# Optimization experiments

Hardware: AMD Instinct MI355X
Metric: run time of the kernel (lower is better)

Reference implementation:

```python
import jax, jax.numpy as jnp
import numpy as np

N_NODES = 50000
N_EDGES = 800000
IN_CH, HID_CH, OUT_CH = 128, 128, 64


def gcn_conv(x, edge_index, edge_weight, W, b, n_nodes):
    """PyG GCNConv: h = D^-1/2 (A + I) D^-1/2 (x @ W) + b, with weighted edges."""
    src, dst = edge_index[0], edge_index[1]
    loop = jnp.arange(n_nodes)
    src_l = jnp.concatenate([src, loop])               # [E+N]
    dst_l = jnp.concatenate([dst, loop])               # [E+N]
    w_l = jnp.concatenate([edge_weight, jnp.ones((n_nodes,), x.dtype)])
    deg = jax.ops.segment_sum(w_l, dst_l, num_segments=n_nodes)  # weighted in-degree incl. self-loop
    dinv = jnp.where(deg > 0, jax.lax.rsqrt(deg), 0.0)
    norm = dinv[src_l] * w_l * dinv[dst_l]             # [E+N]
    h = x @ W                                          # [N, out]
    msg = h[src_l] * norm[:, None]                     # [E+N, out] gather + scale
    out = jax.ops.segment_sum(msg, dst_l, num_segments=n_nodes)  # scatter-add
    return out + b


def setup_inputs() -> dict:
    key = jax.random.key(0)
    k = jax.random.split(key, 8)
    x = jax.random.normal(k[0], (N_NODES, IN_CH), dtype=jnp.float32)
    edge_index = jax.random.randint(k[1], (2, N_EDGES), 0, N_NODES, dtype=jnp.int64)
    edge_weight = jax.random.uniform(k[2], (N_EDGES,), dtype=jnp.float32)
    s1 = 1.0 / np.sqrt(IN_CH)
    s2 = 1.0 / np.sqrt(HID_CH)
    W1 = jax.random.uniform(k[3], (IN_CH, HID_CH), jnp.float32, -s1, s1)
    b1 = jnp.zeros((HID_CH,), jnp.float32)
    W2 = jax.random.uniform(k[4], (HID_CH, OUT_CH), jnp.float32, -s2, s2)
    b2 = jnp.zeros((OUT_CH,), jnp.float32)
    return {"x": x, "edge_index": edge_index, "edge_weight": edge_weight,
            "W1": W1, "b1": b1, "W2": W2, "b2": b2}


def reference(x, edge_index, edge_weight, W1, b1, W2, b2):
    n = x.shape[0]
    h = jax.nn.relu(gcn_conv(x, edge_index, edge_weight, W1, b1, n))
    # dropout(p=0.5) is identity in eval mode
    h = gcn_conv(h, edge_index, edge_weight, W2, b2, n)
    return jax.nn.log_softmax(h, axis=1)
```

## Files before the change

kernel.cpp:

```cpp
#include <hip/hip_runtime.h>
#include <math.h>

static constexpr int CH_IN  = 128;
static constexpr int CH_HID = 128;
static constexpr int CH_OUT = 64;
static constexpr int NBLK1  = 256;

typedef __attribute__((ext_vector_type(8))) short bf16x8;
typedef __attribute__((ext_vector_type(4))) float f32x4;


__device__ __forceinline__ float bf2f(unsigned short u) {
    return __uint_as_float(((unsigned int)u) << 16);
}
__device__ __forceinline__ unsigned short f2bf(float f) {
    unsigned int u = __float_as_uint(f);
    u = (u + 0x7fffu + ((u >> 16) & 1u)) >> 16;
    return (unsigned short)u;
}
__device__ __forceinline__ unsigned int pack2(float lo, float hi) {
    return (unsigned int)f2bf(lo) | ((unsigned int)f2bf(hi) << 16);
}
__device__ __forceinline__ void unpack2(unsigned int u, float& lo, float& hi) {
    lo = __uint_as_float(u << 16);
    hi = __uint_as_float(u & 0xffff0000u);
}
__device__ __forceinline__ unsigned int relu2(unsigned int u) {
    unsigned int m = 0;
    if (!(u & 0x8000u)) m |= 0xffffu;
    if (!(u & 0x80000000u)) m |= 0xffff0000u;
    return u & m;
}

__device__ __forceinline__ void gacc(const uint4* __restrict__ hp, int stride, int ci,
                                     int s, float nm, float* acc) {
    uint4 v = hp[(size_t)s * stride + ci];
    float lo, hi;
    unpack2(v.x, lo, hi); acc[0] = fmaf(lo, nm, acc[0]); acc[1] = fmaf(hi, nm, acc[1]);
    unpack2(v.y, lo, hi); acc[2] = fmaf(lo, nm, acc[2]); acc[3] = fmaf(hi, nm, acc[3]);
    unpack2(v.z, lo, hi); acc[4] = fmaf(lo, nm, acc[4]); acc[5] = fmaf(hi, nm, acc[5]);
    unpack2(v.w, lo, hi); acc[6] = fmaf(lo, nm, acc[6]); acc[7] = fmaf(hi, nm, acc[7]);
}

__device__ __forceinline__ int block_incl_scan_256(int v, int lane, int wid) {
    __shared__ int wtot[4];
    int s = v;
    #pragma unroll
    for (int off = 1; off < 64; off <<= 1) {
        int t = __shfl_up(s, off, 64);
        if (lane >= off) s += t;
    }
    if (lane == 63) wtot[wid] = s;
    __syncthreads();
    int woff = 0;
    for (int j = 0; j < wid; ++j) woff += wtot[j];
    return s + woff;
}


__global__ void k_setup(const float* __restrict__ W1, unsigned short* __restrict__ w1t,
                        const float* __restrict__ W2, unsigned short* __restrict__ w2t) {
    int j = blockIdx.x * blockDim.x + threadIdx.x;
    if (j < CH_HID * 128) {
        int c = j >> 7, k = j & 127;
        w1t[(size_t)c * 128 + k] = f2bf(W1[(size_t)k * CH_HID + c]);
        return;
    }
    j -= CH_HID * 128;
    if (j < CH_OUT * 128) {
        int c = j >> 7, k = j & 127;
        w2t[(size_t)c * 128 + k] = f2bf(W2[(size_t)k * CH_OUT + c]);
    }
}


template<int COLS, bool RELU_IN, typename TIN>
__device__ __forceinline__ void gemm_body(const TIN* __restrict__ X,
                                          const unsigned short* __restrict__ Wt,
                                          unsigned short* __restrict__ H, int N, int blk) {
    constexpr int NCT = COLS / 16;
    __shared__ unsigned short As[64 * 136];
    const int tid = threadIdx.x;
    const int lane = tid & 63, wv = tid >> 6;
    const int row0 = blk * 64;

    if constexpr (sizeof(TIN) == 4) {
        #pragma unroll
        for (int j = 0; j < 8; ++j) {
            int f = j * 256 + tid;
            int row = f >> 5, col = (f & 31) * 4;
            float4 v = make_float4(0.f, 0.f, 0.f, 0.f);
            if (row0 + row < N)
                v = *reinterpret_cast<const float4*>((const float*)X + (size_t)(row0 + row) * CH_IN + col);
            uint2 p;
            p.x = pack2(v.x, v.y);
            p.y = pack2(v.z, v.w);
            *reinterpret_cast<uint2*>(&As[row * 136 + col]) = p;
        }
    } else {
        #pragma unroll
        for (int j = 0; j < 4; ++j) {
            int f = j * 256 + tid;
            int row = f >> 4, col = (f & 15) * 8;
            uint4 v = make_uint4(0u, 0u, 0u, 0u);
            if (row0 + row < N) {
                v = *reinterpret_cast<const uint4*>((const unsigned short*)X + (size_t)(row0 + row) * CH_IN + col);
                if (RELU_IN) {
                    v.x = relu2(v.x); v.y = relu2(v.y);
                    v.z = relu2(v.z); v.w = relu2(v.w);
                }
            }
            *reinterpret_cast<uint4*>(&As[row * 136 + col]) = v;
        }
    }
    __syncthreads();

    const int rw0  = wv * 16;
    const int arow = rw0 + (lane & 15);
    const int kgrp = (lane >> 4) * 8;
    f32x4 acc[NCT];
    #pragma unroll
    for (int c = 0; c < NCT; ++c) acc[c] = f32x4{0.f, 0.f, 0.f, 0.f};

    #pragma unroll
    for (int kk = 0; kk < 4; ++kk) {
        bf16x8 af = *reinterpret_cast<const bf16x8*>(&As[arow * 136 + kk * 32 + kgrp]);
        #pragma unroll
        for (int ct = 0; ct < NCT; ++ct) {
            bf16x8 bf = *reinterpret_cast<const bf16x8*>(
                Wt + (size_t)(ct * 16 + (lane & 15)) * 128 + kk * 32 + kgrp);
            acc[ct] = __builtin_amdgcn_mfma_f32_16x16x32_bf16(af, bf, acc[ct], 0, 0, 0);
        }
    }

    const int orow0 = row0 + rw0 + (lane >> 4) * 4;
    const int ocol  = lane & 15;
    #pragma unroll
    for (int ct = 0; ct < NCT; ++ct) {
        #pragma unroll
        for (int r = 0; r < 4; ++r) {
            int row = orow0 + r;
            if (row < N) H[(size_t)row * COLS + ct * 16 + ocol] = f2bf(acc[ct][r]);
        }
    }
}


__global__ void __launch_bounds__(256) k_fat(
        const float* __restrict__ x, const unsigned short* __restrict__ w1t,
        unsigned short* __restrict__ h1, int N, int nbg,
        const int* __restrict__ ei, int* __restrict__ cnt_bk, int E, int nbk, int epb) {
    __shared__ int bcnt[256];
    if ((int)blockIdx.x < nbg) {
        gemm_body<CH_HID, false, float>(x, w1t, h1, N, blockIdx.x);
    } else {
        const int b = blockIdx.x - nbg;
        const int tid = threadIdx.x;
        bcnt[tid] = 0;
        __syncthreads();
        const int e0 = b * epb, e1 = min(E, e0 + epb);
        for (int e = e0 + tid; e < e1; e += 256)
            atomicAdd(&bcnt[ei[E + e] >> 8], 1);
        __syncthreads();
        if (tid < nbk) cnt_bk[tid * NBLK1 + b] = bcnt[tid];
    }
}

template<int COLS, bool RELU_IN, typename TIN>
__global__ void __launch_bounds__(256) k_gemm_mfma(const TIN* __restrict__ X,
        const unsigned short* __restrict__ Wt, unsigned short* __restrict__ H, int N) {
    gemm_body<COLS, RELU_IN, TIN>(X, Wt, H, N, blockIdx.x);
}


__global__ void k_bscan(const int* __restrict__ cnt_bk, int* __restrict__ off_bk,
                        int* __restrict__ btot) {
    const int k = blockIdx.x, tid = threadIdx.x, lane = tid & 63, wid = tid >> 6;
    int c = cnt_bk[k * NBLK1 + tid];
    int incl = block_incl_scan_256(c, lane, wid);
    off_bk[k * NBLK1 + tid] = incl - c;
    if (tid == 255) btot[k] = incl;
}


__global__ void k_bbase(const int* __restrict__ btot, int* __restrict__ gbase,
                        int* __restrict__ rowptr, int nbk, int E) {
    const int tid = threadIdx.x, lane = tid & 63, wid = tid >> 6;
    int v = (tid < nbk) ? btot[tid] : 0;
    int incl = block_incl_scan_256(v, lane, wid);
    if (tid < nbk) gbase[tid] = incl - v;
    if (tid == 0) { gbase[nbk] = E; rowptr[0] = 0; }
}


__global__ void k_scat(const int* __restrict__ ei, const float* __restrict__ w,
                       const int* __restrict__ gbase, const int* __restrict__ off_bk,
                       uint2* __restrict__ ebuck, int E, int nbk, int epb) {
    __shared__ int lcur[256];
    const int b = blockIdx.x, tid = threadIdx.x;
    if (tid < nbk) lcur[tid] = gbase[tid] + off_bk[tid * NBLK1 + b];
    __syncthreads();
    const int e0 = b * epb, e1 = min(E, e0 + epb);
    for (int e = e0 + tid; e < e1; e += 256) {
        unsigned int s = (unsigned int)ei[e];
        unsigned int d = (unsigned int)ei[E + e];
        int pos = atomicAdd(&lcur[d >> 8], 1);
        ebuck[pos] = make_uint2((d << 16) | s, __float_as_uint(w[e]));
    }
}


__global__ void k_csr(const uint2* __restrict__ ebuck, const int* __restrict__ gbase,
                      int* __restrict__ rowptr, float* __restrict__ dinv,
                      int2* __restrict__ epack, int N) {
    __shared__ int ncnt[256];
    __shared__ float wsm[256];
    const int k = blockIdx.x, tid = threadIdx.x, lane = tid & 63, wid = tid >> 6;
    const int ebeg = gbase[k], eend = gbase[k + 1];
    ncnt[tid] = 0; wsm[tid] = 0.f;
    __syncthreads();
    for (int i = ebeg + tid; i < eend; i += 256) {
        uint2 p = ebuck[i];
        int dl = (p.x >> 16) & 255;
        atomicAdd(&ncnt[dl], 1);
        atomicAdd(&wsm[dl], __uint_as_float(p.y));
    }
    __syncthreads();
    int c = ncnt[tid];
    int incl = block_incl_scan_256(c, lane, wid);
    const int nd = k * 256 + tid;
    if (nd < N) {
        rowptr[nd + 1] = ebeg + incl;
        dinv[nd] = rsqrtf(1.0f + wsm[tid]);
    }
    __syncthreads();
    ncnt[tid] = ebeg + incl - c;
    __syncthreads();
    for (int i = ebeg + tid; i < eend; i += 256) {
        uint2 p = ebuck[i];
        int dl = (p.x >> 16) & 255;
        int pos = atomicAdd(&ncnt[dl], 1);
        epack[pos] = make_int2((int)(p.x & 0xFFFFu), (int)p.y);
    }
}


__global__ void k_agg128(const int* __restrict__ rowptr, const int2* __restrict__ epack,
                         const float* __restrict__ dinv, const unsigned short* __restrict__ h,
                         const float* __restrict__ b, unsigned short* __restrict__ out, int N) {
    const int node = (blockIdx.x * blockDim.x + threadIdx.x) >> 6;
    const int lane = threadIdx.x & 63;
    if (node >= N) return;
    const int beg = rowptr[node], end = rowptr[node + 1];
    const float dd = dinv[node];
    const int g  = lane >> 4;
    const int ci = lane & 15;
    const uint4* hp = (const uint4*)h;

    float acc[8];
    #pragma unroll
    for (int q = 0; q < 8; ++q) acc[q] = 0.f;

    for (int i0 = beg; i0 < end; i0 += 64) {
        const int m = min(64, end - i0);
        int s_l = 0; float nm_l = 0.f;
        if (lane < m) {
            int2 p = epack[i0 + lane];
            s_l = p.x;
            nm_l = __int_as_float(p.y) * dinv[p.x];
        }
        int j = 0;
        for (; j + 16 <= m; j += 16) {
            #pragma unroll
            for (int kk = 0; kk < 4; ++kk) {
                int idx = j + 4 * kk + g;
                int   s  = __shfl(s_l, idx, 64);
                float nm = __shfl(nm_l, idx, 64);
                gacc(hp, 16, ci, s, nm, acc);
            }
        }
        for (; j < m; j += 4) {
            int idx = j + g;
            int   s  = __shfl(s_l, idx, 64);
            float nm = __shfl(nm_l, idx, 64);
            gacc(hp, 16, ci, s, nm, acc);
        }
    }
    #pragma unroll
    for (int q = 0; q < 8; ++q) {
        acc[q] += __shfl_xor(acc[q], 16, 64);
        acc[q] += __shfl_xor(acc[q], 32, 64);
    }
    uint4 hv = hp[(size_t)node * 16 + ci];
    float hn[8];
    unpack2(hv.x, hn[0], hn[1]); unpack2(hv.y, hn[2], hn[3]);
    unpack2(hv.z, hn[4], hn[5]); unpack2(hv.w, hn[6], hn[7]);
    float4 b0 = *reinterpret_cast<const float4*>(b + 8 * ci);
    float4 b1v = *reinterpret_cast<const float4*>(b + 8 * ci + 4);
    const float bb[8] = {b0.x, b0.y, b0.z, b0.w, b1v.x, b1v.y, b1v.z, b1v.w};
    float res[8];
    #pragma unroll
    for (int q = 0; q < 8; ++q)
        res[q] = fmaf(acc[q], dd, fmaf(hn[q], dd * dd, bb[q]));
    if (g == 0) {
        uint4 o;
        o.x = pack2(res[0], res[1]); o.y = pack2(res[2], res[3]);
        o.z = pack2(res[4], res[5]); o.w = pack2(res[6], res[7]);
        ((uint4*)out)[(size_t)node * 16 + ci] = o;
    }
}

__global__ void k_agg64(const int* __restrict__ rowptr, const int2* __restrict__ epack,
                        const float* __restrict__ dinv, const unsigned short* __restrict__ h,
                        const float* __restrict__ b, float* __restrict__ out, int N) {
    const int node = (blockIdx.x * blockDim.x + threadIdx.x) >> 6;
    const int lane = threadIdx.x & 63;
    if (node >= N) return;
    const int beg = rowptr[node], end = rowptr[node + 1];
    const float dd = dinv[node];
    const int g  = lane >> 3;
    const int ci = lane & 7;
    const uint4* hp = (const uint4*)h;

    float acc[8];
    #pragma unroll
    for (int q = 0; q < 8; ++q) acc[q] = 0.f;

    for (int i0 = beg; i0 < end; i0 += 64) {
        const int m = min(64, end - i0);
        int s_l = 0; float nm_l = 0.f;
        if (lane < m) {
            int2 p = epack[i0 + lane];
            s_l = p.x;
            nm_l = __int_as_float(p.y) * dinv[p.x];
        }
        int j = 0;
        for (; j + 32 <= m; j += 32) {
            #pragma unroll
            for (int kk = 0; kk < 4; ++kk) {
                int idx = j + 8 * kk + g;
                int   s  = __shfl(s_l, idx, 64);
                float nm = __shfl(nm_l, idx, 64);
                gacc(hp, 8, ci, s, nm, acc);
            }
        }
        for (; j < m; j += 8) {
            int idx = j + g;
            int   s  = __shfl(s_l, idx, 64);
            float nm = __shfl(nm_l, idx, 64);
            gacc(hp, 8, ci, s, nm, acc);
        }
    }
    #pragma unroll
    for (int q = 0; q < 8; ++q) {
        acc[q] += __shfl_xor(acc[q], 8, 64);
        acc[q] += __shfl_xor(acc[q], 16, 64);
        acc[q] += __shfl_xor(acc[q], 32, 64);
    }
    uint4 hv = hp[(size_t)node * 8 + ci];
    float hn[8];
    unpack2(hv.x, hn[0], hn[1]); unpack2(hv.y, hn[2], hn[3]);
    unpack2(hv.z, hn[4], hn[5]); unpack2(hv.w, hn[6], hn[7]);
    float4 b0 = *reinterpret_cast<const float4*>(b + 8 * ci);
    float4 b1v = *reinterpret_cast<const float4*>(b + 8 * ci + 4);
    const float bb[8] = {b0.x, b0.y, b0.z, b0.w, b1v.x, b1v.y, b1v.z, b1v.w};
    float res[8];
    #pragma unroll
    for (int q = 0; q < 8; ++q)
        res[q] = fmaf(acc[q], dd, fmaf(hn[q], dd * dd, bb[q]));

    float mx = res[0];
    #pragma unroll
    for (int q = 1; q < 8; ++q) mx = fmaxf(mx, res[q]);
    mx = fmaxf(mx, __shfl_xor(mx, 1, 64));
    mx = fmaxf(mx, __shfl_xor(mx, 2, 64));
    mx = fmaxf(mx, __shfl_xor(mx, 4, 64));
    float sm = 0.f;
    #pragma unroll
    for (int q = 0; q < 8; ++q) sm += expf(res[q] - mx);
    sm += __shfl_xor(sm, 1, 64);
    sm += __shfl_xor(sm, 2, 64);
    sm += __shfl_xor(sm, 4, 64);
    float lse = mx + logf(sm);
    if (g == 0) {
        float4 o0 = make_float4(res[0] - lse, res[1] - lse, res[2] - lse, res[3] - lse);
        float4 o1 = make_float4(res[4] - lse, res[5] - lse, res[6] - lse, res[7] - lse);
        *reinterpret_cast<float4*>(out + (size_t)node * 64 + 8 * ci)     = o0;
        *reinterpret_cast<float4*>(out + (size_t)node * 64 + 8 * ci + 4) = o1;
    }
}

extern "C" void kernel_launch(void* const* d_in, const int* in_sizes, int n_in,
                              void* d_out, int out_size, void* d_ws, size_t ws_size,
                              hipStream_t stream) {
    const float* x  = (const float*)d_in[0];
    const int*   ei = (const int*)d_in[1];
    const float* w  = (const float*)d_in[2];
    const float* W1 = (const float*)d_in[3];
    const float* b1 = (const float*)d_in[4];
    const float* W2 = (const float*)d_in[5];
    const float* b2 = (const float*)d_in[6];
    float* out = (float*)d_out;

    const int N = in_sizes[0] / CH_IN;
    const int E = in_sizes[2];
    const int NBK = (N + 255) >> 8;
    const int EPB = (E + NBLK1 - 1) / NBLK1;

    float* ws0   = (float*)d_ws;
    float* ws    = ws0;
    float* dinv  = ws;               ws += N;
    int*   rowptr= (int*)ws;         ws += (N + 2);
    int*   cnt_bk= (int*)ws;         ws += 256 * NBLK1;
    int*   off_bk= (int*)ws;         ws += 256 * NBLK1;
    int*   btot  = (int*)ws;         ws += 256;
    int*   gbase = (int*)ws;         ws += 260;
    uint2* ebuck = (uint2*)ws;       ws += (size_t)2 * E;
    int2*  epack = (int2*)ws;        ws += (size_t)2 * E;
    { size_t off = (size_t)(ws - ws0) & 3; if (off) ws += 4 - off; }
    unsigned short* w1t  = (unsigned short*)ws;  ws += (size_t)CH_HID * 128 / 2;
    unsigned short* w2t  = (unsigned short*)ws;  ws += (size_t)CH_OUT * 128 / 2;
    unsigned short* h1   = (unsigned short*)ws;  ws += (size_t)N * CH_HID / 2;
    unsigned short* out1 = (unsigned short*)ws;  ws += (size_t)N * CH_HID / 2;
    unsigned short* h2   = (unsigned short*)ws;  ws += (size_t)N * CH_OUT / 2;

    const int B = 256;

    k_setup<<<(CH_HID * 128 + CH_OUT * 128 + B - 1) / B, B, 0, stream>>>(W1, w1t, W2, w2t);

    {
        const int nbg = (N + 63) / 64;
        k_fat<<<nbg + NBLK1, B, 0, stream>>>(x, w1t, h1, N, nbg, ei, cnt_bk, E, NBK, EPB);
    }

    k_bscan<<<NBK, 256, 0, stream>>>(cnt_bk, off_bk, btot);
    k_bbase<<<1, 256, 0, stream>>>(btot, gbase, rowptr, NBK, E);

    k_scat<<<NBLK1, 256, 0, stream>>>(ei, w, gbase, off_bk, ebuck, E, NBK, EPB);

    k_csr<<<NBK, 256, 0, stream>>>(ebuck, gbase, rowptr, dinv, epack, N);

    k_agg128<<<(N * 64 + B - 1) / B, B, 0, stream>>>(rowptr, epack, dinv, h1, b1, out1, N);

    k_gemm_mfma<CH_OUT, true, unsigned short><<<(N + 63) / 64, 256, 0, stream>>>(out1, w2t, h2, N);

    k_agg64<<<(N * 64 + B - 1) / B, B, 0, stream>>>(rowptr, epack, dinv, h2, b2, out, N);
}
```

Measured before the change: 144.6 us.

## Fold weight transpose into GEMM and merge scatter with layer-1 GEMM

Removes the separate weight-setup kernel: each GEMM block now converts and transposes W into shared memory itself. The bucket-base scan kernel is removed by recomputing the small scan of bucket totals inside each scatter block and each CSR block. The edge-scatter step now runs in the same launch as the layer-1 GEMM, while the edge count runs alone first. The aim is fewer kernel launches and better overlap of the GEMM with the edge scatter. The cost is that every GEMM block redundantly converts W and uses more shared memory, which may lower occupancy.

Result: faster. 127.1 us (-12.1%).

```diff
diff --git a/kernel.cpp b/kernel.cpp
--- a/kernel.cpp
+++ b/kernel.cpp
@@ -58,31 +58,23 @@
 }
 
 
-__global__ void k_setup(const float* __restrict__ W1, unsigned short* __restrict__ w1t,
-                        const float* __restrict__ W2, unsigned short* __restrict__ w2t) {
-    int j = blockIdx.x * blockDim.x + threadIdx.x;
-    if (j < CH_HID * 128) {
-        int c = j >> 7, k = j & 127;
-        w1t[(size_t)c * 128 + k] = f2bf(W1[(size_t)k * CH_HID + c]);
-        return;
-    }
-    j -= CH_HID * 128;
-    if (j < CH_OUT * 128) {
-        int c = j >> 7, k = j & 127;
-        w2t[(size_t)c * 128 + k] = f2bf(W2[(size_t)k * CH_OUT + c]);
-    }
-}
-
-
 template<int COLS, bool RELU_IN, typename TIN>
 __device__ __forceinline__ void gemm_body(const TIN* __restrict__ X,
-                                          const unsigned short* __restrict__ Wt,
+                                          const float* __restrict__ W,
                                           unsigned short* __restrict__ H, int N, int blk) {
     constexpr int NCT = COLS / 16;
     __shared__ unsigned short As[64 * 136];
+    __shared__ unsigned short Wt[COLS * 136];
     const int tid = threadIdx.x;
     const int lane = tid & 63, wv = tid >> 6;
     const int row0 = blk * 64;
+
+    #pragma unroll
+    for (int it = 0; it < (128 * COLS) / 256; ++it) {
+        int f = it * 256 + tid;
+        int k = f / COLS, c = f & (COLS - 1);
+        Wt[c * 136 + k] = f2bf(W[f]);
+    }
 
     if constexpr (sizeof(TIN) == 4) {
         #pragma unroll
@@ -128,7 +120,7 @@
         #pragma unroll
         for (int ct = 0; ct < NCT; ++ct) {
             bf16x8 bf = *reinterpret_cast<const bf16x8*>(
-                Wt + (size_t)(ct * 16 + (lane & 15)) * 128 + kk * 32 + kgrp);
+                &Wt[(ct * 16 + (lane & 15)) * 136 + kk * 32 + kgrp]);
             acc[ct] = __builtin_amdgcn_mfma_f32_16x16x32_bf16(af, bf, acc[ct], 0, 0, 0);
         }
     }
@@ -146,30 +138,17 @@
 }
 
 
-__global__ void __launch_bounds__(256) k_fat(
-        const float* __restrict__ x, const unsigned short* __restrict__ w1t,
-        unsigned short* __restrict__ h1, int N, int nbg,
-        const int* __restrict__ ei, int* __restrict__ cnt_bk, int E, int nbk, int epb) {
+__global__ void k_count(const int* __restrict__ ei, int* __restrict__ cnt_bk,
+                        int E, int nbk, int epb) {
     __shared__ int bcnt[256];
-    if ((int)blockIdx.x < nbg) {
-        gemm_body<CH_HID, false, float>(x, w1t, h1, N, blockIdx.x);
-    } else {
-        const int b = blockIdx.x - nbg;
-        const int tid = threadIdx.x;
-        bcnt[tid] = 0;
-        __syncthreads();
-        const int e0 = b * epb, e1 = min(E, e0 + epb);
-        for (int e = e0 + tid; e < e1; e += 256)
-            atomicAdd(&bcnt[ei[E + e] >> 8], 1);
-        __syncthreads();
-        if (tid < nbk) cnt_bk[tid * NBLK1 + b] = bcnt[tid];
-    }
-}
-
-template<int COLS, bool RELU_IN, typename TIN>
-__global__ void __launch_bounds__(256) k_gemm_mfma(const TIN* __restrict__ X,
-        const unsigned short* __restrict__ Wt, unsigned short* __restrict__ H, int N) {
-    gemm_body<COLS, RELU_IN, TIN>(X, Wt, H, N, blockIdx.x);
+    const int b = blockIdx.x, tid = threadIdx.x;
+    bcnt[tid] = 0;
+    __syncthreads();
+    const int e0 = b * epb, e1 = min(E, e0 + epb);
+    for (int e = e0 + tid; e < e1; e += 256)
+        atomicAdd(&bcnt[ei[E + e] >> 8], 1);
+    __syncthreads();
+    if (tid < nbk) cnt_bk[tid * NBLK1 + b] = bcnt[tid];
 }
 
 
@@ -183,42 +162,52 @@
 }
 
 
-__global__ void k_bbase(const int* __restrict__ btot, int* __restrict__ gbase,
-                        int* __restrict__ rowptr, int nbk, int E) {
-    const int tid = threadIdx.x, lane = tid & 63, wid = tid >> 6;
-    int v = (tid < nbk) ? btot[tid] : 0;
-    int incl = block_incl_scan_256(v, lane, wid);
-    if (tid < nbk) gbase[tid] = incl - v;
-    if (tid == 0) { gbase[nbk] = E; rowptr[0] = 0; }
-}
-
-
-__global__ void k_scat(const int* __restrict__ ei, const float* __restrict__ w,
-                       const int* __restrict__ gbase, const int* __restrict__ off_bk,
-                       uint2* __restrict__ ebuck, int E, int nbk, int epb) {
-    __shared__ int lcur[256];
-    const int b = blockIdx.x, tid = threadIdx.x;
-    if (tid < nbk) lcur[tid] = gbase[tid] + off_bk[tid * NBLK1 + b];
-    __syncthreads();
-    const int e0 = b * epb, e1 = min(E, e0 + epb);
-    for (int e = e0 + tid; e < e1; e += 256) {
-        unsigned int s = (unsigned int)ei[e];
-        unsigned int d = (unsigned int)ei[E + e];
-        int pos = atomicAdd(&lcur[d >> 8], 1);
-        ebuck[pos] = make_uint2((d << 16) | s, __float_as_uint(w[e]));
-    }
-}
-
-
-__global__ void k_csr(const uint2* __restrict__ ebuck, const int* __restrict__ gbase,
+__global__ void __launch_bounds__(256) k_fat(
+        const float* __restrict__ x, const float* __restrict__ W1,
+        unsigned short* __restrict__ h1, int N, int nbg,
+        const int* __restrict__ ei, const float* __restrict__ w,
+        const int* __restrict__ btot, const int* __restrict__ off_bk,
+        uint2* __restrict__ ebuck, int E, int nbk, int epb) {
+    if ((int)blockIdx.x < nbg) {
+        gemm_body<CH_HID, false, float>(x, W1, h1, N, blockIdx.x);
+    } else {
+        __shared__ int lcur[256];
+        const int b = blockIdx.x - nbg;
+        const int tid = threadIdx.x, lane = tid & 63, wid = tid >> 6;
+        int v = (tid < nbk) ? btot[tid] : 0;
+        int incl = block_incl_scan_256(v, lane, wid);
+        if (tid < nbk) lcur[tid] = (incl - v) + off_bk[tid * NBLK1 + b];
+        __syncthreads();
+        const int e0 = b * epb, e1 = min(E, e0 + epb);
+        for (int e = e0 + tid; e < e1; e += 256) {
+            unsigned int s = (unsigned int)ei[e];
+            unsigned int d = (unsigned int)ei[E + e];
+            int pos = atomicAdd(&lcur[d >> 8], 1);
+            ebuck[pos] = make_uint2((d << 16) | s, __float_as_uint(w[e]));
+        }
+    }
+}
+
+template<int COLS, bool RELU_IN, typename TIN>
+__global__ void __launch_bounds__(256) k_gemm_mfma(const TIN* __restrict__ X,
+        const float* __restrict__ W, unsigned short* __restrict__ H, int N) {
+    gemm_body<COLS, RELU_IN, TIN>(X, W, H, N, blockIdx.x);
+}
+
+
+__global__ void k_csr(const uint2* __restrict__ ebuck, const int* __restrict__ btot,
                       int* __restrict__ rowptr, float* __restrict__ dinv,
-                      int2* __restrict__ epack, int N) {
+                      int2* __restrict__ epack, int N, int nbk) {
     __shared__ int ncnt[256];
     __shared__ float wsm[256];
+    __shared__ int ebeg_s, eend_s;
     const int k = blockIdx.x, tid = threadIdx.x, lane = tid & 63, wid = tid >> 6;
-    const int ebeg = gbase[k], eend = gbase[k + 1];
+    int v = (tid < nbk) ? btot[tid] : 0;
+    int incl0 = block_incl_scan_256(v, lane, wid);
+    if (tid == k) { ebeg_s = incl0 - v; eend_s = incl0; }
     ncnt[tid] = 0; wsm[tid] = 0.f;
     __syncthreads();
+    const int ebeg = ebeg_s, eend = eend_s;
     for (int i = ebeg + tid; i < eend; i += 256) {
         uint2 p = ebuck[i];
         int dl = (p.x >> 16) & 255;
@@ -233,6 +222,7 @@
         rowptr[nd + 1] = ebeg + incl;
         dinv[nd] = rsqrtf(1.0f + wsm[tid]);
     }
+    if (k == 0 && tid == 0) rowptr[0] = 0;
     __syncthreads();
     ncnt[tid] = ebeg + incl - c;
     __syncthreads();
@@ -414,35 +404,30 @@
     int*   cnt_bk= (int*)ws;         ws += 256 * NBLK1;
     int*   off_bk= (int*)ws;         ws += 256 * NBLK1;
     int*   btot  = (int*)ws;         ws += 256;
-    int*   gbase = (int*)ws;         ws += 260;
     uint2* ebuck = (uint2*)ws;       ws += (size_t)2 * E;
     int2*  epack = (int2*)ws;        ws += (size_t)2 * E;
     { size_t off = (size_t)(ws - ws0) & 3; if (off) ws += 4 - off; }
-    unsigned short* w1t  = (unsigned short*)ws;  ws += (size_t)CH_HID * 128 / 2;
-    unsigned short* w2t  = (unsigned short*)ws;  ws += (size_t)CH_OUT * 128 / 2;
     unsigned short* h1   = (unsigned short*)ws;  ws += (size_t)N * CH_HID / 2;
     unsigned short* out1 = (unsigned short*)ws;  ws += (size_t)N * CH_HID / 2;
     unsigned short* h2   = (unsigned short*)ws;  ws += (size_t)N * CH_OUT / 2;
 
     const int B = 256;
 
-    k_setup<<<(CH_HID * 128 + CH_OUT * 128 + B - 1) / B, B, 0, stream>>>(W1, w1t, W2, w2t);
+    k_count<<<NBLK1, B, 0, stream>>>(ei, cnt_bk, E, NBK, EPB);
+
+    k_bscan<<<NBK, 256, 0, stream>>>(cnt_bk, off_bk, btot);
 
     {
         const int nbg = (N + 63) / 64;
-        k_fat<<<nbg + NBLK1, B, 0, stream>>>(x, w1t, h1, N, nbg, ei, cnt_bk, E, NBK, EPB);
-    }
-
-    k_bscan<<<NBK, 256, 0, stream>>>(cnt_bk, off_bk, btot);
-    k_bbase<<<1, 256, 0, stream>>>(btot, gbase, rowptr, NBK, E);
-
-    k_scat<<<NBLK1, 256, 0, stream>>>(ei, w, gbase, off_bk, ebuck, E, NBK, EPB);
-
-    k_csr<<<NBK, 256, 0, stream>>>(ebuck, gbase, rowptr, dinv, epack, N);
+        k_fat<<<nbg + NBLK1, B, 0, stream>>>(x, W1, h1, N, nbg,
+                                             ei, w, btot, off_bk, ebuck, E, NBK, EPB);
+    }
+
+    k_csr<<<NBK, 256, 0, stream>>>(ebuck, btot, rowptr, dinv, epack, N, NBK);
 
     k_agg128<<<(N * 64 + B - 1) / B, B, 0, stream>>>(rowptr, epack, dinv, h1, b1, out1, N);
 
-    k_gemm_mfma<CH_OUT, true, unsigned short><<<(N + 63) / 64, 256, 0, stream>>>(out1, w2t, h2, N);
+    k_gemm_mfma<CH_OUT, true, unsigned short><<<(N + 63) / 64, 256, 0, stream>>>(out1, W2, h2, N);
 
     k_agg64<<<(N * 64 + B - 1) / B, B, 0, stream>>>(rowptr, epack, dinv, h2, b2, out, N);
 }
```

## Reorder CSR build stages and fold bucket-base scan into consumers

Applied to the files above, without the earlier changes.

Merges the weight conversion into the edge-count kernel and moves the edge scatter into the fat kernel alongside the first GEMM. The single-block base scan is dropped: each scatter block and each CSR block recomputes the prefix over bucket totals itself. This cuts two kernel launches and their serialization gaps, and lets the scatter overlap the GEMM. In exchange, the scan work is repeated in every block.

Result: faster. 136.9 us (-5.4%).

```diff
diff --git a/kernel.cpp b/kernel.cpp
--- a/kernel.cpp
+++ b/kernel.cpp
@@ -55,22 +55,6 @@
     int woff = 0;
     for (int j = 0; j < wid; ++j) woff += wtot[j];
     return s + woff;
-}
-
-
-__global__ void k_setup(const float* __restrict__ W1, unsigned short* __restrict__ w1t,
-                        const float* __restrict__ W2, unsigned short* __restrict__ w2t) {
-    int j = blockIdx.x * blockDim.x + threadIdx.x;
-    if (j < CH_HID * 128) {
-        int c = j >> 7, k = j & 127;
-        w1t[(size_t)c * 128 + k] = f2bf(W1[(size_t)k * CH_HID + c]);
-        return;
-    }
-    j -= CH_HID * 128;
-    if (j < CH_OUT * 128) {
-        int c = j >> 7, k = j & 127;
-        w2t[(size_t)c * 128 + k] = f2bf(W2[(size_t)k * CH_OUT + c]);
-    }
 }
 
 
@@ -146,16 +130,14 @@
 }
 
 
-__global__ void __launch_bounds__(256) k_fat(
-        const float* __restrict__ x, const unsigned short* __restrict__ w1t,
-        unsigned short* __restrict__ h1, int N, int nbg,
-        const int* __restrict__ ei, int* __restrict__ cnt_bk, int E, int nbk, int epb) {
+__global__ void k_count(const int* __restrict__ ei, int* __restrict__ cnt_bk,
+                        int E, int nbk, int epb,
+                        const float* __restrict__ W1, unsigned short* __restrict__ w1t,
+                        const float* __restrict__ W2, unsigned short* __restrict__ w2t) {
     __shared__ int bcnt[256];
-    if ((int)blockIdx.x < nbg) {
-        gemm_body<CH_HID, false, float>(x, w1t, h1, N, blockIdx.x);
-    } else {
-        const int b = blockIdx.x - nbg;
-        const int tid = threadIdx.x;
+    const int tid = threadIdx.x;
+    if ((int)blockIdx.x < NBLK1) {
+        const int b = blockIdx.x;
         bcnt[tid] = 0;
         __syncthreads();
         const int e0 = b * epb, e1 = min(E, e0 + epb);
@@ -163,13 +145,19 @@
             atomicAdd(&bcnt[ei[E + e] >> 8], 1);
         __syncthreads();
         if (tid < nbk) cnt_bk[tid * NBLK1 + b] = bcnt[tid];
-    }
-}
-
-template<int COLS, bool RELU_IN, typename TIN>
-__global__ void __launch_bounds__(256) k_gemm_mfma(const TIN* __restrict__ X,
-        const unsigned short* __restrict__ Wt, unsigned short* __restrict__ H, int N) {
-    gemm_body<COLS, RELU_IN, TIN>(X, Wt, H, N, blockIdx.x);
+    } else {
+        int j = (blockIdx.x - NBLK1) * 256 + tid;
+        if (j < CH_HID * 128) {
+            int c = j >> 7, k = j & 127;
+            w1t[(size_t)c * 128 + k] = f2bf(W1[(size_t)k * CH_HID + c]);
+            return;
+        }
+        j -= CH_HID * 128;
+        if (j < CH_OUT * 128) {
+            int c = j >> 7, k = j & 127;
+            w2t[(size_t)c * 128 + k] = f2bf(W2[(size_t)k * CH_OUT + c]);
+        }
+    }
 }
 
 
@@ -183,42 +171,52 @@
 }
 
 
-__global__ void k_bbase(const int* __restrict__ btot, int* __restrict__ gbase,
-                        int* __restrict__ rowptr, int nbk, int E) {
-    const int tid = threadIdx.x, lane = tid & 63, wid = tid >> 6;
-    int v = (tid < nbk) ? btot[tid] : 0;
-    int incl = block_incl_scan_256(v, lane, wid);
-    if (tid < nbk) gbase[tid] = incl - v;
-    if (tid == 0) { gbase[nbk] = E; rowptr[0] = 0; }
-}
-
-
-__global__ void k_scat(const int* __restrict__ ei, const float* __restrict__ w,
-                       const int* __restrict__ gbase, const int* __restrict__ off_bk,
-                       uint2* __restrict__ ebuck, int E, int nbk, int epb) {
-    __shared__ int lcur[256];
-    const int b = blockIdx.x, tid = threadIdx.x;
-    if (tid < nbk) lcur[tid] = gbase[tid] + off_bk[tid * NBLK1 + b];
-    __syncthreads();
-    const int e0 = b * epb, e1 = min(E, e0 + epb);
-    for (int e = e0 + tid; e < e1; e += 256) {
-        unsigned int s = (unsigned int)ei[e];
-        unsigned int d = (unsigned int)ei[E + e];
-        int pos = atomicAdd(&lcur[d >> 8], 1);
-        ebuck[pos] = make_uint2((d << 16) | s, __float_as_uint(w[e]));
-    }
-}
-
-
-__global__ void k_csr(const uint2* __restrict__ ebuck, const int* __restrict__ gbase,
+__global__ void __launch_bounds__(256) k_fat(
+        const float* __restrict__ x, const unsigned short* __restrict__ w1t,
+        unsigned short* __restrict__ h1, int N, int nbg,
+        const int* __restrict__ ei, const float* __restrict__ w,
+        const int* __restrict__ btot, const int* __restrict__ off_bk,
+        uint2* __restrict__ ebuck, int E, int nbk, int epb) {
+    if ((int)blockIdx.x < nbg) {
+        gemm_body<CH_HID, false, float>(x, w1t, h1, N, blockIdx.x);
+    } else {
+        __shared__ int lcur[256];
+        const int b = blockIdx.x - nbg;
+        const int tid = threadIdx.x, lane = tid & 63, wid = tid >> 6;
+        int v = (tid < nbk) ? btot[tid] : 0;
+        int incl = block_incl_scan_256(v, lane, wid);
+        if (tid < nbk) lcur[tid] = (incl - v) + off_bk[tid * NBLK1 + b];
+        __syncthreads();
+        const int e0 = b * epb, e1 = min(E, e0 + epb);
+        for (int e = e0 + tid; e < e1; e += 256) {
+            unsigned int s = (unsigned int)ei[e];
+            unsigned int d = (unsigned int)ei[E + e];
+            int pos = atomicAdd(&lcur[d >> 8], 1);
+            ebuck[pos] = make_uint2((d << 16) | s, __float_as_uint(w[e]));
+        }
+    }
+}
+
+template<int COLS, bool RELU_IN, typename TIN>
+__global__ void __launch_bounds__(256) k_gemm_mfma(const TIN* __restrict__ X,
+        const unsigned short* __restrict__ Wt, unsigned short* __restrict__ H, int N) {
+    gemm_body<COLS, RELU_IN, TIN>(X, Wt, H, N, blockIdx.x);
+}
+
+
+__global__ void k_csr(const uint2* __restrict__ ebuck, const int* __restrict__ btot,
                       int* __restrict__ rowptr, float* __restrict__ dinv,
-                      int2* __restrict__ epack, int N) {
+                      int2* __restrict__ epack, int N, int nbk) {
     __shared__ int ncnt[256];
     __shared__ float wsm[256];
+    __shared__ int ebeg_s, eend_s;
     const int k = blockIdx.x, tid = threadIdx.x, lane = tid & 63, wid = tid >> 6;
-    const int ebeg = gbase[k], eend = gbase[k + 1];
+    int v = (tid < nbk) ? btot[tid] : 0;
+    int incl0 = block_incl_scan_256(v, lane, wid);
+    if (tid == k) { ebeg_s = incl0 - v; eend_s = incl0; }
     ncnt[tid] = 0; wsm[tid] = 0.f;
     __syncthreads();
+    const int ebeg = ebeg_s, eend = eend_s;
     for (int i = ebeg + tid; i < eend; i += 256) {
         uint2 p = ebuck[i];
         int dl = (p.x >> 16) & 255;
@@ -233,6 +231,7 @@
         rowptr[nd + 1] = ebeg + incl;
         dinv[nd] = rsqrtf(1.0f + wsm[tid]);
     }
+    if (k == 0 && tid == 0) rowptr[0] = 0;
     __syncthreads();
     ncnt[tid] = ebeg + incl - c;
     __syncthreads();
@@ -406,6 +405,7 @@
     const int E = in_sizes[2];
     const int NBK = (N + 255) >> 8;
     const int EPB = (E + NBLK1 - 1) / NBLK1;
+    const int WTB = (CH_HID * 128 + CH_OUT * 128 + 255) / 256;
 
     float* ws0   = (float*)d_ws;
     float* ws    = ws0;
@@ -414,7 +414,6 @@
     int*   cnt_bk= (int*)ws;         ws += 256 * NBLK1;
     int*   off_bk= (int*)ws;         ws += 256 * NBLK1;
     int*   btot  = (int*)ws;         ws += 256;
-    int*   gbase = (int*)ws;         ws += 260;
     uint2* ebuck = (uint2*)ws;       ws += (size_t)2 * E;
     int2*  epack = (int2*)ws;        ws += (size_t)2 * E;
     { size_t off = (size_t)(ws - ws0) & 3; if (off) ws += 4 - off; }
@@ -426,19 +425,17 @@
 
     const int B = 256;
 
-    k_setup<<<(CH_HID * 128 + CH_OUT * 128 + B - 1) / B, B, 0, stream>>>(W1, w1t, W2, w2t);
+    k_count<<<NBLK1 + WTB, B, 0, stream>>>(ei, cnt_bk, E, NBK, EPB, W1, w1t, W2, w2t);
+
+    k_bscan<<<NBK, 256, 0, stream>>>(cnt_bk, off_bk, btot);
 
     {
         const int nbg = (N + 63) / 64;
-        k_fat<<<nbg + NBLK1, B, 0, stream>>>(x, w1t, h1, N, nbg, ei, cnt_bk, E, NBK, EPB);
-    }
-
-    k_bscan<<<NBK, 256, 0, stream>>>(cnt_bk, off_bk, btot);
-    k_bbase<<<1, 256, 0, stream>>>(btot, gbase, rowptr, NBK, E);
-
-    k_scat<<<NBLK1, 256, 0, stream>>>(ei, w, gbase, off_bk, ebuck, E, NBK, EPB);
-
-    k_csr<<<NBK, 256, 0, stream>>>(ebuck, gbase, rowptr, dinv, epack, N);
+        k_fat<<<nbg + NBLK1, B, 0, stream>>>(x, w1t, h1, N, nbg,
+                                             ei, w, btot, off_bk, ebuck, E, NBK, EPB);
+    }
+
+    k_csr<<<NBK, 256, 0, stream>>>(ebuck, btot, rowptr, dinv, epack, N, NBK);
 
     k_agg128<<<(N * 64 + B - 1) / B, B, 0, stream>>>(rowptr, epack, dinv, h1, b1, out1, N);
 
```
